# Optimization experiments

Hardware: AMD Instinct MI355X
Metric: run time of the kernel (lower is better)

Reference implementation:

```python
import jax, jax.numpy as jnp
import numpy as np

B, T, D, H, E, TOP_K = 2, 2048, 1024, 4096, 8, 2


def setup_inputs() -> dict:
    key = jax.random.key(0)
    ks = jax.random.split(key, 7)
    s_d = 1.0 / np.sqrt(D)
    s_h = 1.0 / np.sqrt(H)
    return {
        "x": jax.random.normal(ks[0], (B, T, D), dtype=jnp.float32),
        "gate_w": jax.random.uniform(ks[1], (D, E), minval=-s_d, maxval=s_d, dtype=jnp.float32),
        "gate_b": jax.random.uniform(ks[2], (E,), minval=-s_d, maxval=s_d, dtype=jnp.float32),
        "w1": jax.random.uniform(ks[3], (E, D, H), minval=-s_d, maxval=s_d, dtype=jnp.float32),
        "b1": jax.random.uniform(ks[4], (E, H), minval=-s_d, maxval=s_d, dtype=jnp.float32),
        "w2": jax.random.uniform(ks[5], (E, H, D), minval=-s_h, maxval=s_h, dtype=jnp.float32),
        "b2": jax.random.uniform(ks[6], (E, D), minval=-s_h, maxval=s_h, dtype=jnp.float32),
    }


def reference(x, gate_w, gate_b, w1, b1, w2, b2):
    Bsz, Tn, Din = x.shape
    x_flat = x.reshape(-1, Din)                       # [N, D]
    N = x_flat.shape[0]
    gating_logits = x_flat @ gate_w + gate_b          # [N, E]
    weights, indices = jax.lax.top_k(gating_logits, TOP_K)
    weights = jax.nn.softmax(weights, axis=-1).astype(x.dtype)
    # scatter top-k weights into dense dispatch tensor [N, E]
    dispatch = jnp.zeros((N, E), dtype=x.dtype).at[jnp.arange(N)[:, None], indices].set(weights)
    # NOTE: faithful to original - gate weight multiplies the expert INPUT
    # and again the expert OUTPUT (double weighting through the GELU MLP).
    dispatched_x = dispatch[:, :, None] * x_flat[:, None, :]       # [N, E, D]
    h = jax.nn.gelu(jnp.einsum('ned,edh->neh', dispatched_x, w1) + b1, approximate=False)
    expert_out = jnp.einsum('neh,ehd->ned', h, w2) + b2            # [N, E, D]
    combined = jnp.sum(dispatch[:, :, None] * expert_out, axis=1)  # [N, D]
    final = combined.reshape(Bsz, Tn, -1)
    return final, gating_logits
```

## Files before the change

kernel.cpp:

```cpp
#include <hip/hip_runtime.h>
#include <hip/hip_bf16.h>
#include <math.h>

#define NTOK 4096
#define DDIM 1024
#define HDIM 4096
#define NEXP 8
#define CAP  4096
#define ROWCAP 9216
#define MAXTILES 72

typedef __attribute__((ext_vector_type(8))) short short8;
typedef __attribute__((ext_vector_type(4))) float f32x4;

#define GLOAD_LDS16(g, l) __builtin_amdgcn_global_load_lds( \
    (const __attribute__((address_space(1))) void*)(g),     \
    (__attribute__((address_space(3))) void*)(l), 16, 0, 0)

__global__ __launch_bounds__(256) void gating_kernel(
    const float* __restrict__ x, const float* __restrict__ gw,
    const float* __restrict__ gb, float* __restrict__ logits_out,
    int* __restrict__ counts, int* __restrict__ tok, float* __restrict__ gate,
    int* __restrict__ eA, int* __restrict__ sA, float* __restrict__ gA) {
  int t = blockIdx.x;
  int tid = threadIdx.x;
  float p[NEXP];
#pragma unroll
  for (int e = 0; e < NEXP; ++e) p[e] = 0.f;
  const float* xr = x + (size_t)t * DDIM;
  for (int d = tid; d < DDIM; d += 256) {
    float xv = xr[d];
    const float* wr = gw + (size_t)d * NEXP;
#pragma unroll
    for (int e = 0; e < NEXP; ++e) p[e] += xv * wr[e];
  }
#pragma unroll
  for (int off = 32; off > 0; off >>= 1)
#pragma unroll
    for (int e = 0; e < NEXP; ++e) p[e] += __shfl_xor(p[e], off, 64);
  __shared__ float red[4][NEXP];
  int wave = tid >> 6, lane = tid & 63;
  if (lane == 0)
#pragma unroll
    for (int e = 0; e < NEXP; ++e) red[wave][e] = p[e];
  __syncthreads();
  if (tid < NEXP) {
    float v = red[0][tid] + red[1][tid] + red[2][tid] + red[3][tid] + gb[tid];
    logits_out[(size_t)t * NEXP + tid] = v;
    red[0][tid] = v;
  }
  __syncthreads();
  if (tid == 0) {
    float v[NEXP];
#pragma unroll
    for (int e = 0; e < NEXP; ++e) v[e] = red[0][e];
    int i0 = 0;
#pragma unroll
    for (int e = 1; e < NEXP; ++e) if (v[e] > v[i0]) i0 = e;
    int i1 = (i0 == 0) ? 1 : 0;
#pragma unroll
    for (int e = 0; e < NEXP; ++e) if (e != i0 && v[e] > v[i1]) i1 = e;
    float e1 = expf(v[i1] - v[i0]);
    float s = 1.f + e1;
    float g0 = 1.f / s, g1 = e1 / s;
    int s0 = atomicAdd(&counts[i0], 1);
    tok[i0 * CAP + s0] = t; gate[i0 * CAP + s0] = g0;
    int s1 = atomicAdd(&counts[i1], 1);
    tok[i1 * CAP + s1] = t; gate[i1 * CAP + s1] = g1;
    eA[2 * t] = i0; sA[2 * t] = s0; gA[2 * t] = g0;
    eA[2 * t + 1] = i1; sA[2 * t + 1] = s1; gA[2 * t + 1] = g1;
  }
}

__global__ void sched_kernel(const int* __restrict__ counts, int* __restrict__ poff,
                             int* __restrict__ tileE, int* __restrict__ tileR,
                             int* __restrict__ nTiles) {
  if (threadIdx.x == 0) {
    int acc = 0, nt = 0;
    for (int e = 0; e < NEXP; ++e) {
      poff[e] = acc;
      int tl = (counts[e] + 127) >> 7;
      for (int t = 0; t < tl; ++t) { tileE[nt] = e; tileR[nt] = acc + t * 128; ++nt; }
      acc += tl << 7;
    }
    poff[NEXP] = acc;
    nTiles[0] = nt;
  }
}

__global__ __launch_bounds__(256) void transpose_all(
    const float* __restrict__ w1, const float* __restrict__ w2,
    __hip_bfloat16* __restrict__ wT1, __hip_bfloat16* __restrict__ wT2) {
  __shared__ float tile[64 * 65];
  int id = blockIdx.x;
  const float* inp; __hip_bfloat16* outp; int R, C, bx, by;
  if (id < 8192) {
    int e = id >> 10, rem = id & 1023;
    bx = rem & 63; by = rem >> 6;
    R = 1024; C = 4096;
    inp = w1 + (size_t)e * R * C; outp = wT1 + (size_t)e * R * C;
  } else {
    id -= 8192;
    int e = id >> 10, rem = id & 1023;
    bx = rem & 15; by = rem >> 4;
    R = 4096; C = 1024;
    inp = w2 + (size_t)e * R * C; outp = wT2 + (size_t)e * R * C;
  }
  int c0 = bx * 64, r0 = by * 64;
  int tx = threadIdx.x & 15, ty = threadIdx.x >> 4;
#pragma unroll
  for (int i = 0; i < 64; i += 16) {
    float4 v = *(const float4*)(inp + (size_t)(r0 + ty + i) * C + c0 + tx * 4);
    float* dst = tile + (ty + i) * 65 + tx * 4;
    dst[0] = v.x; dst[1] = v.y; dst[2] = v.z; dst[3] = v.w;
  }
  __syncthreads();
  int c = threadIdx.x >> 3;
  int rb = (threadIdx.x & 7) * 8;
#pragma unroll
  for (int p = 0; p < 2; ++p) {
    int cc = c + p * 32;
    union { unsigned short u[8]; short8 v8; } pk;
#pragma unroll
    for (int j = 0; j < 8; ++j) {
      __hip_bfloat16 h = __float2bfloat16(tile[(rb + j) * 65 + cc]);
      pk.u[j] = *(unsigned short*)&h;
    }
    *(short8*)(outp + (size_t)(c0 + cc) * R + r0 + rb) = pk.v8;
  }
}

__global__ __launch_bounds__(256) void gather_kernel(
    const float* __restrict__ x, const int* __restrict__ counts,
    const int* __restrict__ poff, const int* __restrict__ tok,
    const float* __restrict__ gate, __hip_bfloat16* __restrict__ Xg) {
  int e = blockIdx.y, r = blockIdx.x;
  int pc = poff[e + 1] - poff[e];
  if (r >= pc) return;
  int row = poff[e] + r;
  int tid = threadIdx.x;
  __hip_bfloat16* orow = Xg + (size_t)row * DDIM;
  if (r < counts[e]) {
    int t = tok[e * CAP + r];
    float g = gate[e * CAP + r];
    float4 v = ((const float4*)(x + (size_t)t * DDIM))[tid];
    union { unsigned short u[4]; uint2 q; } pk;
    __hip_bfloat16 h0 = __float2bfloat16(v.x * g);
    __hip_bfloat16 h1 = __float2bfloat16(v.y * g);
    __hip_bfloat16 h2 = __float2bfloat16(v.z * g);
    __hip_bfloat16 h3 = __float2bfloat16(v.w * g);
    pk.u[0] = *(unsigned short*)&h0; pk.u[1] = *(unsigned short*)&h1;
    pk.u[2] = *(unsigned short*)&h2; pk.u[3] = *(unsigned short*)&h3;
    ((uint2*)orow)[tid] = pk.q;
  } else {
    uint2 z; z.x = 0; z.y = 0;
    ((uint2*)orow)[tid] = z;
  }
}

template <int EPI>
__global__ __launch_bounds__(256) void moe_gemm(
    const __hip_bfloat16* __restrict__ A, const __hip_bfloat16* __restrict__ B,
    const float* __restrict__ bias, __hip_bfloat16* __restrict__ Hout,
    float* __restrict__ Pout, const int* __restrict__ tileE,
    const int* __restrict__ tileR, const int* __restrict__ nTiles,
    int K, int Nn) {
  int f = (blockIdx.z * gridDim.y + blockIdx.y) * gridDim.x + blockIdx.x;
  int xcd = f & 7, seq = f >> 3;
  int ct, ty, kz;
  if (EPI == 0) {
    ct = xcd * 4 + (seq & 3); ty = seq >> 2; kz = 0;
  } else {
    ct = xcd; ty = seq % MAXTILES; kz = seq / MAXTILES;
  }
  if (ty >= nTiles[0]) return;
  int e = tileE[ty];
  int rowBase = tileR[ty];
  int colBase = ct * 128;

  __shared__ __align__(16) char As[128 * 64];
  __shared__ __align__(16) char Bs[128 * 64];

  const char* Ae = (const char*)A + (size_t)rowBase * K * 2;
  const char* Be = (const char*)B + ((size_t)e * Nn + colBase) * (size_t)K * 2;

  int tid = threadIdx.x;
  int wave = tid >> 6, lane = tid & 63;
  int srow = lane >> 2;
  int cg = (((lane & 3) ^ ((lane >> 3) & 3)) << 4);

  f32x4 acc[4][4] = {};

  int wm = (wave >> 1) * 64, wn = (wave & 1) * 64;
  int frm = lane & 15;
  int fsw = (((lane >> 4) ^ ((lane >> 1) & 3)) << 4);

  int kPer = (EPI == 1) ? (K >> 1) : K;
  int kLo = kz * kPer, kHi = kLo + kPer;

  for (int k0 = kLo; k0 < kHi; k0 += 32) {
    __syncthreads();
#pragma unroll
    for (int c = 0; c < 2; ++c) {
      int ch = wave * 2 + c;
      int r = ch * 16 + srow;
      GLOAD_LDS16(Ae + ((size_t)r * K + k0) * 2 + cg, As + ch * 1024 + lane * 16);
      GLOAD_LDS16(Be + ((size_t)r * K + k0) * 2 + cg, Bs + ch * 1024 + lane * 16);
    }
    __syncthreads();
    short8 af[4], bfr[4];
#pragma unroll
    for (int i = 0; i < 4; ++i) {
      af[i]  = *(const short8*)(As + (wm + i * 16 + frm) * 64 + fsw);
      bfr[i] = *(const short8*)(Bs + (wn + i * 16 + frm) * 64 + fsw);
    }
#pragma unroll
    for (int i = 0; i < 4; ++i)
#pragma unroll
      for (int j = 0; j < 4; ++j)
        acc[i][j] = __builtin_amdgcn_mfma_f32_16x16x32_bf16(af[i], bfr[j], acc[i][j], 0, 0, 0);
  }

  int cq = lane >> 4, cn = lane & 15;
  if (EPI == 0) {
#pragma unroll
    for (int i = 0; i < 4; ++i) {
#pragma unroll
      for (int j = 0; j < 4; ++j) {
        int col = colBase + wn + j * 16 + cn;
        float bv = bias[e * Nn + col];
#pragma unroll
        for (int r = 0; r < 4; ++r) {
          int row = rowBase + wm + i * 16 + cq * 4 + r;
          float v = acc[i][j][r] + bv;
          float z = 1.5957691f * v * (1.0f + 0.044715f * v * v);
          v = v / (1.0f + __expf(-z));
          Hout[(size_t)row * Nn + col] = __float2bfloat16(v);
        }
      }
    }
  } else {
    float* Pp = Pout + ((size_t)kz * ROWCAP + rowBase) * DDIM;
#pragma unroll
    for (int i = 0; i < 4; ++i) {
#pragma unroll
      for (int j = 0; j < 4; ++j) {
        int col = colBase + wn + j * 16 + cn;
#pragma unroll
        for (int r = 0; r < 4; ++r) {
          int row = wm + i * 16 + cq * 4 + r;
          Pp[(size_t)row * DDIM + col] = acc[i][j][r];
        }
      }
    }
  }
}

__global__ __launch_bounds__(256) void combine_kernel(
    const float* __restrict__ P, const float* __restrict__ b2,
    const int* __restrict__ poff, const int* __restrict__ eA,
    const int* __restrict__ sA, const float* __restrict__ gA,
    float* __restrict__ outF) {
  int t = blockIdx.x, c = threadIdx.x;
  int e0 = eA[2 * t], e1 = eA[2 * t + 1];
  int r0 = poff[e0] + sA[2 * t], r1 = poff[e1] + sA[2 * t + 1];
  float g0 = gA[2 * t], g1 = gA[2 * t + 1];
  float4 a0 = ((const float4*)(P + (size_t)r0 * DDIM))[c];
  float4 a1 = ((const float4*)(P + ((size_t)ROWCAP + r0) * DDIM))[c];
  float4 b0 = ((const float4*)(P + (size_t)r1 * DDIM))[c];
  float4 b1 = ((const float4*)(P + ((size_t)ROWCAP + r1) * DDIM))[c];
  float4 bb0 = ((const float4*)(b2 + (size_t)e0 * DDIM))[c];
  float4 bb1 = ((const float4*)(b2 + (size_t)e1 * DDIM))[c];
  float4 o;
  o.x = g0 * (a0.x + a1.x + bb0.x) + g1 * (b0.x + b1.x + bb1.x);
  o.y = g0 * (a0.y + a1.y + bb0.y) + g1 * (b0.y + b1.y + bb1.y);
  o.z = g0 * (a0.z + a1.z + bb0.z) + g1 * (b0.z + b1.z + bb1.z);
  o.w = g0 * (a0.w + a1.w + bb0.w) + g1 * (b0.w + b1.w + bb1.w);
  ((float4*)(outF + (size_t)t * DDIM))[c] = o;
}

extern "C" void kernel_launch(void* const* d_in, const int* in_sizes, int n_in,
                              void* d_out, int out_size, void* d_ws, size_t ws_size,
                              hipStream_t stream) {
  const float* x  = (const float*)d_in[0];
  const float* gw = (const float*)d_in[1];
  const float* gb = (const float*)d_in[2];
  const float* w1 = (const float*)d_in[3];
  const float* b1 = (const float*)d_in[4];
  const float* w2 = (const float*)d_in[5];
  const float* b2 = (const float*)d_in[6];

  float* outF = (float*)d_out;
  float* outL = outF + (size_t)NTOK * DDIM;

  size_t off = 0;
  char* base = (char*)d_ws;
  auto alloc = [&](size_t bytes) {
    void* r = base + off;
    off += (bytes + 255) & ~(size_t)255;
    return r;
  };
  __hip_bfloat16* wT1 = (__hip_bfloat16*)alloc((size_t)NEXP * HDIM * DDIM * 2);
  __hip_bfloat16* Xg  = (__hip_bfloat16*)alloc((size_t)ROWCAP * DDIM * 2);
  __hip_bfloat16* wT2 = (__hip_bfloat16*)alloc((size_t)NEXP * DDIM * HDIM * 2);
  __hip_bfloat16* Hact= (__hip_bfloat16*)alloc((size_t)ROWCAP * HDIM * 2);
  int*   tok    = (int*)alloc((size_t)NEXP * CAP * 4);
  float* gate   = (float*)alloc((size_t)NEXP * CAP * 4);
  int*   eA     = (int*)alloc((size_t)NTOK * 2 * 4);
  int*   sA     = (int*)alloc((size_t)NTOK * 2 * 4);
  float* gA     = (float*)alloc((size_t)NTOK * 2 * 4);
  int*   counts = (int*)alloc(64);
  int*   poff   = (int*)alloc(64);
  int*   tileE  = (int*)alloc(MAXTILES * 4);
  int*   tileR  = (int*)alloc(MAXTILES * 4);
  int*   nTiles = (int*)alloc(64);
  float* P      = (float*)wT1;

  hipMemsetAsync(counts, 0, 64, stream);
  gating_kernel<<<NTOK, 256, 0, stream>>>(x, gw, gb, outL, counts, tok, gate, eA, sA, gA);
  sched_kernel<<<1, 64, 0, stream>>>(counts, poff, tileE, tileR, nTiles);
  transpose_all<<<16384, 256, 0, stream>>>(w1, w2, wT1, wT2);
  gather_kernel<<<dim3(CAP, NEXP), 256, 0, stream>>>(x, counts, poff, tok, gate, Xg);
  moe_gemm<0><<<dim3(HDIM / 128, MAXTILES, 1), 256, 0, stream>>>(
      Xg, wT1, b1, Hact, nullptr, tileE, tileR, nTiles, DDIM, HDIM);
  moe_gemm<1><<<dim3(DDIM / 128, MAXTILES, 2), 256, 0, stream>>>(
      Hact, wT2, b2, nullptr, P, tileE, tileR, nTiles, HDIM, DDIM);
  combine_kernel<<<NTOK, 256, 0, stream>>>(P, b2, poff, eA, sA, gA, outF);
}
```

Before: 715.9 us.

## Enlarge MoE GEMM tiles to 256x128 with double-buffered LDS prefetch

The grouped expert GEMM now uses 512-thread blocks on 256-row by 128-column tiles with a K-step of 64. It double-buffers the A and B tiles in LDS with XOR-swizzled layouts, prefetching the next K-slice by direct global-to-LDS loads while MFMAs run on the current one. It also raises wave priority around the MFMA bursts and splits the A-fragment reads into two halves. The scheduler pads each expert to 256-row tiles, which raises row capacity and may add padded-row work. The aim is to hide global load latency and cut barrier overhead, at the cost of 96KB of LDS and lower occupancy.

```diff
diff --git a/kernel.cpp b/kernel.cpp
--- a/kernel.cpp
+++ b/kernel.cpp
@@ -7,8 +7,8 @@
 #define HDIM 4096
 #define NEXP 8
 #define CAP  4096
-#define ROWCAP 9216
-#define MAXTILES 72
+#define ROWCAP 10240
+#define MAXTILES 40
 
 typedef __attribute__((ext_vector_type(8))) short short8;
 typedef __attribute__((ext_vector_type(4))) float f32x4;
@@ -79,9 +79,9 @@
     int acc = 0, nt = 0;
     for (int e = 0; e < NEXP; ++e) {
       poff[e] = acc;
-      int tl = (counts[e] + 127) >> 7;
-      for (int t = 0; t < tl; ++t) { tileE[nt] = e; tileR[nt] = acc + t * 128; ++nt; }
-      acc += tl << 7;
+      int tl = (counts[e] + 255) >> 8;
+      for (int t = 0; t < tl; ++t) { tileE[nt] = e; tileR[nt] = acc + t * 256; ++nt; }
+      acc += tl << 8;
     }
     poff[NEXP] = acc;
     nTiles[0] = nt;
@@ -159,7 +159,7 @@
 }
 
 template <int EPI>
-__global__ __launch_bounds__(256) void moe_gemm(
+__global__ __launch_bounds__(512) void moe_gemm(
     const __hip_bfloat16* __restrict__ A, const __hip_bfloat16* __restrict__ B,
     const float* __restrict__ bias, __hip_bfloat16* __restrict__ Hout,
     float* __restrict__ Pout, const int* __restrict__ tileE,
@@ -178,47 +178,108 @@
   int rowBase = tileR[ty];
   int colBase = ct * 128;
 
-  __shared__ __align__(16) char As[128 * 64];
-  __shared__ __align__(16) char Bs[128 * 64];
+  __shared__ __align__(16) char LA[65536];
+  __shared__ __align__(16) char LB[32768];
 
   const char* Ae = (const char*)A + (size_t)rowBase * K * 2;
   const char* Be = (const char*)B + ((size_t)e * Nn + colBase) * (size_t)K * 2;
 
   int tid = threadIdx.x;
-  int wave = tid >> 6, lane = tid & 63;
-  int srow = lane >> 2;
-  int cg = (((lane & 3) ^ ((lane >> 3) & 3)) << 4);
+  int lane = tid & 63, wave = tid >> 6;
+  int wm = (wave >> 1) * 64, wn = (wave & 1) * 64;
+  int frm = lane & 15, g = lane >> 4;
+
+  int sr = tid >> 3;
+  int sch = (tid & 7) ^ (sr & 7);
+  const char* aS = Ae + (size_t)sr * K * 2 + sch * 16;
+  const char* bS = Be + (size_t)sr * K * 2 + sch * 16;
+  char* dA = LA + tid * 16;
+  char* dB = LB + tid * 16;
+  size_t rstep = (size_t)64 * K * 2;
+
+  int f7 = frm & 7;
+  int sl0 = (g ^ f7) << 4;
+  int sl1 = ((4 + g) ^ f7) << 4;
+  const char* rA = LA + (wm + frm) * 128;
+  const char* rB = LB + (wn + frm) * 128;
 
   f32x4 acc[4][4] = {};
-
-  int wm = (wave >> 1) * 64, wn = (wave & 1) * 64;
-  int frm = lane & 15;
-  int fsw = (((lane >> 4) ^ ((lane >> 1) & 3)) << 4);
-
   int kPer = (EPI == 1) ? (K >> 1) : K;
-  int kLo = kz * kPer, kHi = kLo + kPer;
-
-  for (int k0 = kLo; k0 < kHi; k0 += 32) {
-    __syncthreads();
-#pragma unroll
-    for (int c = 0; c < 2; ++c) {
-      int ch = wave * 2 + c;
-      int r = ch * 16 + srow;
-      GLOAD_LDS16(Ae + ((size_t)r * K + k0) * 2 + cg, As + ch * 1024 + lane * 16);
-      GLOAD_LDS16(Be + ((size_t)r * K + k0) * 2 + cg, Bs + ch * 1024 + lane * 16);
-    }
-    __syncthreads();
-    short8 af[4], bfr[4];
-#pragma unroll
-    for (int i = 0; i < 4; ++i) {
-      af[i]  = *(const short8*)(As + (wm + i * 16 + frm) * 64 + fsw);
-      bfr[i] = *(const short8*)(Bs + (wn + i * 16 + frm) * 64 + fsw);
-    }
-#pragma unroll
-    for (int i = 0; i < 4; ++i)
-#pragma unroll
-      for (int j = 0; j < 4; ++j)
-        acc[i][j] = __builtin_amdgcn_mfma_f32_16x16x32_bf16(af[i], bfr[j], acc[i][j], 0, 0, 0);
+  int kLo = kz * kPer;
+  int NT = kPer >> 6;
+
+  {
+    const char* a = aS + (size_t)kLo * 2;
+    const char* b = bS + (size_t)kLo * 2;
+#pragma unroll
+    for (int j = 0; j < 4; ++j) GLOAD_LDS16(a + j * rstep, dA + j * 8192);
+#pragma unroll
+    for (int j = 0; j < 2; ++j) GLOAD_LDS16(b + j * rstep, dB + j * 8192);
+  }
+  asm volatile("s_waitcnt vmcnt(0)" ::: "memory");
+  __builtin_amdgcn_sched_barrier(0);
+  __builtin_amdgcn_s_barrier();
+
+  for (int t = 0; t < NT; ++t) {
+    int p = t & 1;
+    if (t + 1 < NT) {
+      const char* a = aS + (size_t)(kLo + (t + 1) * 64) * 2;
+      const char* b = bS + (size_t)(kLo + (t + 1) * 64) * 2;
+      char* da = dA + (p ^ 1) * 32768;
+      char* db = dB + (p ^ 1) * 16384;
+#pragma unroll
+      for (int j = 0; j < 4; ++j) GLOAD_LDS16(a + j * rstep, da + j * 8192);
+#pragma unroll
+      for (int j = 0; j < 2; ++j) GLOAD_LDS16(b + j * rstep, db + j * 8192);
+    }
+    const char* Ab = rA + p * 32768;
+    const char* Bb = rB + p * 16384;
+    short8 af[2][2], bf[4][2], ag[2][2];
+#pragma unroll
+    for (int i = 0; i < 2; ++i) {
+      af[i][0] = *(const short8*)(Ab + i * 2048 + sl0);
+      af[i][1] = *(const short8*)(Ab + i * 2048 + sl1);
+    }
+#pragma unroll
+    for (int j = 0; j < 4; ++j) {
+      bf[j][0] = *(const short8*)(Bb + j * 2048 + sl0);
+      bf[j][1] = *(const short8*)(Bb + j * 2048 + sl1);
+    }
+    __builtin_amdgcn_s_barrier();
+    asm volatile("s_waitcnt lgkmcnt(0)" ::: "memory");
+    __builtin_amdgcn_sched_barrier(0);
+    __builtin_amdgcn_s_setprio(1);
+#pragma unroll
+    for (int ks = 0; ks < 2; ++ks)
+#pragma unroll
+      for (int i = 0; i < 2; ++i)
+#pragma unroll
+        for (int j = 0; j < 4; ++j)
+          acc[i][j] = __builtin_amdgcn_mfma_f32_16x16x32_bf16(
+              af[i][ks], bf[j][ks], acc[i][j], 0, 0, 0);
+    __builtin_amdgcn_s_setprio(0);
+    __builtin_amdgcn_s_barrier();
+#pragma unroll
+    for (int i = 0; i < 2; ++i) {
+      ag[i][0] = *(const short8*)(Ab + (i + 2) * 2048 + sl0);
+      ag[i][1] = *(const short8*)(Ab + (i + 2) * 2048 + sl1);
+    }
+    __builtin_amdgcn_s_barrier();
+    asm volatile("s_waitcnt lgkmcnt(0)" ::: "memory");
+    __builtin_amdgcn_sched_barrier(0);
+    __builtin_amdgcn_s_setprio(1);
+#pragma unroll
+    for (int ks = 0; ks < 2; ++ks)
+#pragma unroll
+      for (int i = 0; i < 2; ++i)
+#pragma unroll
+        for (int j = 0; j < 4; ++j)
+          acc[i + 2][j] = __builtin_amdgcn_mfma_f32_16x16x32_bf16(
+              ag[i][ks], bf[j][ks], acc[i + 2][j], 0, 0, 0);
+    __builtin_amdgcn_s_setprio(0);
+    asm volatile("s_waitcnt vmcnt(0)" ::: "memory");
+    __builtin_amdgcn_sched_barrier(0);
+    __builtin_amdgcn_s_barrier();
   }
 
   int cq = lane >> 4, cn = lane & 15;
@@ -321,9 +382,9 @@
   sched_kernel<<<1, 64, 0, stream>>>(counts, poff, tileE, tileR, nTiles);
   transpose_all<<<16384, 256, 0, stream>>>(w1, w2, wT1, wT2);
   gather_kernel<<<dim3(CAP, NEXP), 256, 0, stream>>>(x, counts, poff, tok, gate, Xg);
-  moe_gemm<0><<<dim3(HDIM / 128, MAXTILES, 1), 256, 0, stream>>>(
+  moe_gemm<0><<<dim3(HDIM / 128, MAXTILES, 1), 512, 0, stream>>>(
       Xg, wT1, b1, Hact, nullptr, tileE, tileR, nTiles, DDIM, HDIM);
-  moe_gemm<1><<<dim3(DDIM / 128, MAXTILES, 2), 256, 0, stream>>>(
+  moe_gemm<1><<<dim3(DDIM / 128, MAXTILES, 2), 512, 0, stream>>>(
       Hact, wT2, b2, nullptr, P, tileE, tileR, nTiles, HDIM, DDIM);
   combine_kernel<<<NTOK, 256, 0, stream>>>(P, b2, poff, eA, sA, gA, outF);
 }
```

New measurement: 760.9 us. +6.3%, slower.
